# Performance work log

Measured on AMD Instinct MI355X. Metric: run time of the kernel, lower is better.

The kernel has to match this reference:

```python
import math
import jax, jax.numpy as jnp
import numpy as np

L, B, E, NDIM = 4096, 4, 1024, 16


def setup_inputs() -> dict:
    key = jax.random.key(0)
    ks = jax.random.split(key, 6)
    x = jax.random.normal(ks[0], (L, B, E), dtype=jnp.float32)
    alpha = jax.random.normal(ks[1], (2 * E, NDIM, 1), dtype=jnp.float32) * 0.2
    delta = jax.random.normal(ks[2], (2 * E, NDIM, 1), dtype=jnp.float32) * 0.2
    # beta init: N(0, 0.02) + alternating +-1 along ndim
    val = np.ones((NDIM, 1), dtype=np.float32)
    val[1::2] = -1.0
    beta = jax.random.normal(ks[3], (2 * E, NDIM, 1), dtype=jnp.float32) * 0.02 + jnp.asarray(val)
    gamma = jax.random.normal(ks[4], (2 * E, NDIM), dtype=jnp.float32)
    omega = jax.random.normal(ks[5], (E,), dtype=jnp.float32)
    return {"x": x, "alpha": alpha, "delta": delta, "beta": beta, "gamma": gamma, "omega": omega}


def reference(x, alpha, delta, beta, gamma, omega):
    seq_len, bsz, embed_dim = x.shape
    ndim = alpha.shape[1]
    scale = math.sqrt(1.0 / ndim)

    residual = x * omega  # (L, B, E)
    xc = jnp.transpose(x, (1, 2, 0))  # (B, E, L)

    a = jax.nn.sigmoid(alpha)
    d = jax.nn.sigmoid(delta)
    q = 1.0 - a * d          # (2E, ndim, 1)
    p = a * beta             # (2E, ndim, 1)

    t = jnp.arange(seq_len, dtype=x.dtype)          # (L,)
    vander = t[None, None, :] * jnp.log(q)          # (2E, ndim, L)
    kernel = p * jnp.exp(vander)                    # (2E, ndim, L)
    k = jnp.einsum('dnl,dn->dl', kernel, gamma * scale)  # (2E, L)

    fft_len = 2 * seq_len  # seq_len + kernel_size (truncation=None)
    k1, k2 = k[:embed_dim], k[embed_dim:]
    # bidirectional + shift: causal part padded right, flipped anti-causal padded left
    kb = jnp.pad(k1, ((0, 0), (0, seq_len))) + jnp.pad(k2[:, ::-1], ((0, 0), (seq_len, 0)))  # (E, 2L)

    k_f = jnp.fft.rfft(kb, n=fft_len)   # (E, L+1) complex
    x_f = jnp.fft.rfft(xc, n=fft_len)   # (B, E, L+1) complex
    out = jnp.fft.irfft(x_f * k_f, n=fft_len)[..., :seq_len]  # (B, E, L)
    out = out.astype(x.dtype)

    return jax.nn.silu(jnp.transpose(out, (2, 0, 1)) + residual)  # (L, B, E)
```

## Files before the change

kernel.cpp:

```cpp
#include <hip/hip_runtime.h>
#include <hip/hip_fp16.h>
#include <math.h>

#define L_  4096
#define B_  4
#define E_  1024
#define ND  16
#define CK  64
#define NC  (L_/CK)
#define BE  (B_*E_)
#define COLS (BE*ND)
#define CW  8

#define OFF_Q   0
#define OFF_W   (2*E_*ND)
#define OFF_QC  (2*2*E_*ND)
#define OFF_FS  (3*2*E_*ND)
#define OFF_GR  (OFF_FS + (size_t)NC*COLS)

__device__ __forceinline__ float sigm(float x){ return 1.0f/(1.0f+__expf(-x)); }

__global__ void k_params(const float* __restrict__ al,
                         const float* __restrict__ de,
                         const float* __restrict__ be,
                         const float* __restrict__ ga,
                         float* __restrict__ ws){
    int i = blockIdx.x*256 + threadIdx.x;
    float a = sigm(al[i]);
    float d = sigm(de[i]);
    float q = 1.0f - a*d;
    float w = a*be[i]*ga[i]*0.25f;
    float qc = q;
    #pragma unroll
    for(int k=0;k<6;k++) qc *= qc;
    ws[OFF_Q+i]=q; ws[OFF_W+i]=w; ws[OFF_QC+i]=qc;
}

__global__ __launch_bounds__(256) void k_summ(const float* __restrict__ x,
                                              float* __restrict__ ws){
    int bid = blockIdx.x;
    int c  = bid >> 4;
    int b  = (bid >> 2) & 3;
    int eg = bid & 3;
    int e  = eg*256 + threadIdx.x;
    const float* Q = ws + OFF_Q;
    float qf[ND], qb[ND], F[ND], G[ND];
    #pragma unroll
    for(int n=0;n<ND;n++){
        qf[n]=Q[e*ND+n]; qb[n]=Q[(E_+e)*ND+n]; F[n]=0.f; G[n]=0.f;
    }
    const float* xp = x + (size_t)(c*CK)*BE + b*E_ + e;
    #pragma unroll 16
    for(int i=0;i<CK;i++){
        float xa = xp[(size_t)i*BE];
        float xb = xp[(size_t)(CK-1-i)*BE];
        #pragma unroll
        for(int n=0;n<ND;n++){
            F[n]=fmaf(qf[n],F[n],xa);
            G[n]=fmaf(qb[n],G[n],xb);
        }
    }
    int col = (b*E_+e)*ND;
    float* Fp = ws + OFF_FS + (size_t)c*COLS + col;
    float* Gp = ws + OFF_GR + (size_t)c*COLS + col;
    #pragma unroll
    for(int n=0;n<ND;n++){ Fp[n]=F[n]; Gp[n]=G[n]; }
}

__global__ __launch_bounds__(256) void k_out2(const float* __restrict__ x,
                                              const float* __restrict__ om,
                                              const float* __restrict__ ws,
                                              float* __restrict__ out){
    __shared__ __half part[CK*256];
    const int tid = threadIdx.x;
    const int bid = blockIdx.x;
    const int c  = bid >> 4;
    const int b  = (bid >> 2) & 3;
    const int eg = bid & 3;
    const int e  = eg*256 + tid;
    const float* Q = ws + OFF_Q;
    const float* W = ws + OFF_W;
    const float omg = om[e];
    const int col = (b*E_+e)*ND;
    const float* xp = x + (size_t)(c*CK)*BE + b*E_ + e;

    {
        float st[ND];
        {
            float pw[ND], qcf[ND];
            #pragma unroll
            for(int n=0;n<ND;n++){ st[n]=0.f; pw[n]=1.f; qcf[n]=ws[OFF_QC+e*ND+n]; }
            int jm = (c < CW) ? c : CW;
            for(int j=1;j<=jm;j++){
                const float4* Fp = (const float4*)(ws + OFF_FS + (size_t)(c-j)*COLS + col);
                #pragma unroll
                for(int v=0;v<4;v++){
                    float4 f = Fp[v];
                    st[4*v+0]=fmaf(pw[4*v+0],f.x,st[4*v+0]);
                    st[4*v+1]=fmaf(pw[4*v+1],f.y,st[4*v+1]);
                    st[4*v+2]=fmaf(pw[4*v+2],f.z,st[4*v+2]);
                    st[4*v+3]=fmaf(pw[4*v+3],f.w,st[4*v+3]);
                }
                #pragma unroll
                for(int n=0;n<ND;n++) pw[n]*=qcf[n];
            }
        }
        float q1[ND], w1[ND];
        #pragma unroll
        for(int n=0;n<ND;n++){ q1[n]=Q[e*ND+n]; w1[n]=W[e*ND+n]; }
        #pragma unroll 4
        for(int i=0;i<CK;i++){
            float xv = xp[(size_t)i*BE];
            float acc = xv*omg;
            #pragma unroll
            for(int n=0;n<ND;n++){ st[n]=fmaf(q1[n],st[n],xv); acc=fmaf(w1[n],st[n],acc); }
            part[i*256+tid] = __float2half_rn(acc);
        }
    }

    {
        float rt[ND];
        {
            float pw[ND], qcb[ND];
            #pragma unroll
            for(int n=0;n<ND;n++){ rt[n]=0.f; pw[n]=1.f; qcb[n]=ws[OFF_QC+(E_+e)*ND+n]; }
            int jm = NC-1-c; if(jm > CW) jm = CW;
            for(int j=1;j<=jm;j++){
                const float4* Gp = (const float4*)(ws + OFF_GR + (size_t)(c+j)*COLS + col);
                #pragma unroll
                for(int v=0;v<4;v++){
                    float4 g = Gp[v];
                    rt[4*v+0]=fmaf(pw[4*v+0],g.x,rt[4*v+0]);
                    rt[4*v+1]=fmaf(pw[4*v+1],g.y,rt[4*v+1]);
                    rt[4*v+2]=fmaf(pw[4*v+2],g.z,rt[4*v+2]);
                    rt[4*v+3]=fmaf(pw[4*v+3],g.w,rt[4*v+3]);
                }
                #pragma unroll
                for(int n=0;n<ND;n++) pw[n]*=qcb[n];
            }
        }
        float q2[ND], w2[ND];
        #pragma unroll
        for(int n=0;n<ND;n++){ q2[n]=Q[(E_+e)*ND+n]; w2[n]=W[(E_+e)*ND+n]; }
        float* op = out + (size_t)(c*CK)*BE + b*E_ + e;
        #pragma unroll 4
        for(int i=CK-1;i>=0;i--){
            float acc = __half2float(part[i*256+tid]);
            #pragma unroll
            for(int n=0;n<ND;n++) acc = fmaf(w2[n], rt[n], acc);
            float z = acc;
            op[(size_t)i*BE] = z / (1.0f + __expf(-z));
            float xv = xp[(size_t)i*BE];
            #pragma unroll
            for(int n=0;n<ND;n++) rt[n]=fmaf(q2[n],rt[n],xv);
        }
    }
}

extern "C" void kernel_launch(void* const* d_in, const int* in_sizes, int n_in,
                              void* d_out, int out_size, void* d_ws, size_t ws_size,
                              hipStream_t stream) {
    const float* x  = (const float*)d_in[0];
    const float* al = (const float*)d_in[1];
    const float* de = (const float*)d_in[2];
    const float* be = (const float*)d_in[3];
    const float* ga = (const float*)d_in[4];
    const float* om = (const float*)d_in[5];
    float* ws = (float*)d_ws;
    float* out = (float*)d_out;

    k_params<<<dim3((2*E_*ND)/256), dim3(256), 0, stream>>>(al, de, be, ga, ws);
    k_summ  <<<dim3(NC*B_*(E_/256)), dim3(256), 0, stream>>>(x, ws);
    k_out2  <<<dim3(NC*B_*(E_/256)), dim3(256), 0, stream>>>(x, om, ws, out);
}
```

Measured before the change: 182.2 us.

## Split state dimension across thread pairs and combine partial sums with shuffles

Each embedding channel is now handled by two threads, each owning half of the 16 SSM state dimensions, which doubles the block count and halves per-thread registers. Partial output contributions are combined with a lane-xor shuffle, and each thread of the pair writes alternating timesteps. Launch bounds request higher occupancy. In exchange, each pair reads x twice, there are extra shuffles per step, and a block-wide sync is added between the forward and backward passes.

```diff
diff --git a/kernel.cpp b/kernel.cpp
--- a/kernel.cpp
+++ b/kernel.cpp
@@ -6,6 +6,7 @@
 #define B_  4
 #define E_  1024
 #define ND  16
+#define NH  8
 #define CK  64
 #define NC  (L_/CK)
 #define BE  (B_*E_)
@@ -36,123 +37,137 @@
     ws[OFF_Q+i]=q; ws[OFF_W+i]=w; ws[OFF_QC+i]=qc;
 }
 
-__global__ __launch_bounds__(256) void k_summ(const float* __restrict__ x,
-                                              float* __restrict__ ws){
-    int bid = blockIdx.x;
-    int c  = bid >> 4;
-    int b  = (bid >> 2) & 3;
-    int eg = bid & 3;
-    int e  = eg*256 + threadIdx.x;
+__global__ __launch_bounds__(256,8) void k_summ(const float* __restrict__ x,
+                                                float* __restrict__ ws){
+    const int bid = blockIdx.x;
+    const int c  = bid >> 5;
+    const int b  = (bid >> 3) & 3;
+    const int eg = bid & 7;
+    const int el = threadIdx.x >> 1;
+    const int h  = threadIdx.x & 1;
+    const int e  = eg*128 + el;
     const float* Q = ws + OFF_Q;
-    float qf[ND], qb[ND], F[ND], G[ND];
+    const int pb = e*ND + NH*h;
+    float qf[NH], qb[NH], F[NH], G[NH];
     #pragma unroll
-    for(int n=0;n<ND;n++){
-        qf[n]=Q[e*ND+n]; qb[n]=Q[(E_+e)*ND+n]; F[n]=0.f; G[n]=0.f;
+    for(int n=0;n<NH;n++){
+        qf[n]=Q[pb+n]; qb[n]=Q[E_*ND+pb+n]; F[n]=0.f; G[n]=0.f;
     }
     const float* xp = x + (size_t)(c*CK)*BE + b*E_ + e;
-    #pragma unroll 16
+    #pragma unroll 8
     for(int i=0;i<CK;i++){
         float xa = xp[(size_t)i*BE];
         float xb = xp[(size_t)(CK-1-i)*BE];
         #pragma unroll
-        for(int n=0;n<ND;n++){
+        for(int n=0;n<NH;n++){
             F[n]=fmaf(qf[n],F[n],xa);
             G[n]=fmaf(qb[n],G[n],xb);
         }
     }
-    int col = (b*E_+e)*ND;
+    const int col = (b*E_+e)*ND + NH*h;
     float* Fp = ws + OFF_FS + (size_t)c*COLS + col;
     float* Gp = ws + OFF_GR + (size_t)c*COLS + col;
     #pragma unroll
-    for(int n=0;n<ND;n++){ Fp[n]=F[n]; Gp[n]=G[n]; }
+    for(int n=0;n<NH;n++){ Fp[n]=F[n]; Gp[n]=G[n]; }
 }
 
-__global__ __launch_bounds__(256) void k_out2(const float* __restrict__ x,
-                                              const float* __restrict__ om,
-                                              const float* __restrict__ ws,
-                                              float* __restrict__ out){
-    __shared__ __half part[CK*256];
+__global__ __launch_bounds__(256,8) void k_out2(const float* __restrict__ x,
+                                                const float* __restrict__ om,
+                                                const float* __restrict__ ws,
+                                                float* __restrict__ out){
+    __shared__ __half part[CK*128];
     const int tid = threadIdx.x;
     const int bid = blockIdx.x;
-    const int c  = bid >> 4;
-    const int b  = (bid >> 2) & 3;
-    const int eg = bid & 3;
-    const int e  = eg*256 + tid;
+    const int c  = bid >> 5;
+    const int b  = (bid >> 3) & 3;
+    const int eg = bid & 7;
+    const int el = tid >> 1;
+    const int h  = tid & 1;
+    const int e  = eg*128 + el;
     const float* Q = ws + OFF_Q;
     const float* W = ws + OFF_W;
-    const float omg = om[e];
-    const int col = (b*E_+e)*ND;
+    const int pb  = e*ND + NH*h;
+    const int col = (b*E_+e)*ND + NH*h;
+    float om_eff = om[e];
+    if(h) om_eff = 0.0f;
     const float* xp = x + (size_t)(c*CK)*BE + b*E_ + e;
 
+    float st[NH];
     {
-        float st[ND];
-        {
-            float pw[ND], qcf[ND];
+        float pw[NH], qcf[NH];
+        #pragma unroll
+        for(int n=0;n<NH;n++){ st[n]=0.f; pw[n]=1.f; qcf[n]=ws[OFF_QC+pb+n]; }
+        int jm = (c < CW) ? c : CW;
+        for(int j=1;j<=jm;j++){
+            const float4* Fp = (const float4*)(ws + OFF_FS + (size_t)(c-j)*COLS + col);
             #pragma unroll
-            for(int n=0;n<ND;n++){ st[n]=0.f; pw[n]=1.f; qcf[n]=ws[OFF_QC+e*ND+n]; }
-            int jm = (c < CW) ? c : CW;
-            for(int j=1;j<=jm;j++){
-                const float4* Fp = (const float4*)(ws + OFF_FS + (size_t)(c-j)*COLS + col);
-                #pragma unroll
-                for(int v=0;v<4;v++){
-                    float4 f = Fp[v];
-                    st[4*v+0]=fmaf(pw[4*v+0],f.x,st[4*v+0]);
-                    st[4*v+1]=fmaf(pw[4*v+1],f.y,st[4*v+1]);
-                    st[4*v+2]=fmaf(pw[4*v+2],f.z,st[4*v+2]);
-                    st[4*v+3]=fmaf(pw[4*v+3],f.w,st[4*v+3]);
-                }
-                #pragma unroll
-                for(int n=0;n<ND;n++) pw[n]*=qcf[n];
+            for(int v=0;v<2;v++){
+                float4 f = Fp[v];
+                st[4*v+0]=fmaf(pw[4*v+0],f.x,st[4*v+0]);
+                st[4*v+1]=fmaf(pw[4*v+1],f.y,st[4*v+1]);
+                st[4*v+2]=fmaf(pw[4*v+2],f.z,st[4*v+2]);
+                st[4*v+3]=fmaf(pw[4*v+3],f.w,st[4*v+3]);
             }
+            #pragma unroll
+            for(int n=0;n<NH;n++) pw[n]*=qcf[n];
         }
-        float q1[ND], w1[ND];
+    }
+    {
+        float q1[NH], w1[NH];
         #pragma unroll
-        for(int n=0;n<ND;n++){ q1[n]=Q[e*ND+n]; w1[n]=W[e*ND+n]; }
+        for(int n=0;n<NH;n++){ q1[n]=Q[pb+n]; w1[n]=W[pb+n]; }
         #pragma unroll 4
         for(int i=0;i<CK;i++){
             float xv = xp[(size_t)i*BE];
-            float acc = xv*omg;
             #pragma unroll
-            for(int n=0;n<ND;n++){ st[n]=fmaf(q1[n],st[n],xv); acc=fmaf(w1[n],st[n],acc); }
-            part[i*256+tid] = __float2half_rn(acc);
+            for(int n=0;n<NH;n++) st[n]=fmaf(q1[n],st[n],xv);
+            float a0 = xv*om_eff, a1 = 0.f;
+            #pragma unroll
+            for(int n=0;n<4;n++){ a0=fmaf(w1[n],st[n],a0); a1=fmaf(w1[n+4],st[n+4],a1); }
+            float ph = a0 + a1;
+            float tot = ph + __shfl_xor(ph, 1);
+            if((i&1)==h) part[i*128+el] = __float2half_rn(tot);
         }
     }
+    __syncthreads();
 
+    float rt[NH];
     {
-        float rt[ND];
-        {
-            float pw[ND], qcb[ND];
+        float pw[NH], qcb[NH];
+        #pragma unroll
+        for(int n=0;n<NH;n++){ rt[n]=0.f; pw[n]=1.f; qcb[n]=ws[OFF_QC+E_*ND+pb+n]; }
+        int jm = NC-1-c; if(jm > CW) jm = CW;
+        for(int j=1;j<=jm;j++){
+            const float4* Gp = (const float4*)(ws + OFF_GR + (size_t)(c+j)*COLS + col);
             #pragma unroll
-            for(int n=0;n<ND;n++){ rt[n]=0.f; pw[n]=1.f; qcb[n]=ws[OFF_QC+(E_+e)*ND+n]; }
-            int jm = NC-1-c; if(jm > CW) jm = CW;
-            for(int j=1;j<=jm;j++){
-                const float4* Gp = (const float4*)(ws + OFF_GR + (size_t)(c+j)*COLS + col);
-                #pragma unroll
-                for(int v=0;v<4;v++){
-                    float4 g = Gp[v];
-                    rt[4*v+0]=fmaf(pw[4*v+0],g.x,rt[4*v+0]);
-                    rt[4*v+1]=fmaf(pw[4*v+1],g.y,rt[4*v+1]);
-                    rt[4*v+2]=fmaf(pw[4*v+2],g.z,rt[4*v+2]);
-                    rt[4*v+3]=fmaf(pw[4*v+3],g.w,rt[4*v+3]);
-                }
-                #pragma unroll
-                for(int n=0;n<ND;n++) pw[n]*=qcb[n];
+            for(int v=0;v<2;v++){
+                float4 g = Gp[v];
+                rt[4*v+0]=fmaf(pw[4*v+0],g.x,rt[4*v+0]);
+                rt[4*v+1]=fmaf(pw[4*v+1],g.y,rt[4*v+1]);
+                rt[4*v+2]=fmaf(pw[4*v+2],g.z,rt[4*v+2]);
+                rt[4*v+3]=fmaf(pw[4*v+3],g.w,rt[4*v+3]);
             }
+            #pragma unroll
+            for(int n=0;n<NH;n++) pw[n]*=qcb[n];
         }
-        float q2[ND], w2[ND];
+    }
+    {
+        float q2[NH], w2[NH];
         #pragma unroll
-        for(int n=0;n<ND;n++){ q2[n]=Q[(E_+e)*ND+n]; w2[n]=W[(E_+e)*ND+n]; }
+        for(int n=0;n<NH;n++){ q2[n]=Q[E_*ND+pb+n]; w2[n]=W[E_*ND+pb+n]; }
         float* op = out + (size_t)(c*CK)*BE + b*E_ + e;
         #pragma unroll 4
         for(int i=CK-1;i>=0;i--){
-            float acc = __half2float(part[i*256+tid]);
+            float b0=0.f, b1=0.f;
             #pragma unroll
-            for(int n=0;n<ND;n++) acc = fmaf(w2[n], rt[n], acc);
-            float z = acc;
-            op[(size_t)i*BE] = z / (1.0f + __expf(-z));
+            for(int n=0;n<4;n++){ b0=fmaf(w2[n],rt[n],b0); b1=fmaf(w2[n+4],rt[n+4],b1); }
+            float bh = b0 + b1;
+            float btot = bh + __shfl_xor(bh, 1);
+            float z = __half2float(part[i*128+el]) + btot;
+            if((i&1)==h) op[(size_t)i*BE] = z / (1.0f + __expf(-z));
             float xv = xp[(size_t)i*BE];
             #pragma unroll
-            for(int n=0;n<ND;n++) rt[n]=fmaf(q2[n],rt[n],xv);
+            for(int n=0;n<NH;n++) rt[n]=fmaf(q2[n],rt[n],xv);
         }
     }
 }
@@ -170,6 +185,6 @@
     float* out = (float*)d_out;
 
     k_params<<<dim3((2*E_*ND)/256), dim3(256), 0, stream>>>(al, de, be, ga, ws);
-    k_summ  <<<dim3(NC*B_*(E_/256)), dim3(256), 0, stream>>>(x, ws);
-    k_out2  <<<dim3(NC*B_*(E_/256)), dim3(256), 0, stream>>>(x, om, ws, out);
+    k_summ  <<<dim3(NC*B_*(E_/128)), dim3(256), 0, stream>>>(x, ws);
+    k_out2  <<<dim3(NC*B_*(E_/128)), dim3(256), 0, stream>>>(x, om, ws, out);
 }
```

Result: slower. 228.5 us (+25.4%).

## Template chunk size to 32 with halved lookback and single-pass summaries

Applied to the files above, without the earlier changes.

Makes the chunk length and cross-chunk lookback window template parameters. The default path now uses 32-step chunks with a 4-chunk lookback when the workspace is large enough, and 64-step chunks with a 4-chunk lookback otherwise. The summary kernel now reads each x value once and computes the reverse-direction state as a power-weighted sum instead of a second strided read. Shorter chunks double the block count and shorten the serial recurrence per thread, but double the summary writes. The reduced lookback truncates the decay tail (q^128 instead of q^512), which could hurt accuracy for slowly decaying channels.

```diff
diff --git a/kernel.cpp b/kernel.cpp
--- a/kernel.cpp
+++ b/kernel.cpp
@@ -6,17 +6,13 @@
 #define B_  4
 #define E_  1024
 #define ND  16
-#define CK  64
-#define NC  (L_/CK)
 #define BE  (B_*E_)
 #define COLS (BE*ND)
-#define CW  8
 
 #define OFF_Q   0
 #define OFF_W   (2*E_*ND)
 #define OFF_QC  (2*2*E_*ND)
 #define OFF_FS  (3*2*E_*ND)
-#define OFF_GR  (OFF_FS + (size_t)NC*COLS)
 
 __device__ __forceinline__ float sigm(float x){ return 1.0f/(1.0f+__expf(-x)); }
 
@@ -24,53 +20,56 @@
                          const float* __restrict__ de,
                          const float* __restrict__ be,
                          const float* __restrict__ ga,
-                         float* __restrict__ ws){
+                         float* __restrict__ ws, int lg){
     int i = blockIdx.x*256 + threadIdx.x;
     float a = sigm(al[i]);
     float d = sigm(de[i]);
     float q = 1.0f - a*d;
     float w = a*be[i]*ga[i]*0.25f;
     float qc = q;
-    #pragma unroll
-    for(int k=0;k<6;k++) qc *= qc;
+    for(int k=0;k<lg;k++) qc *= qc;
     ws[OFF_Q+i]=q; ws[OFF_W+i]=w; ws[OFF_QC+i]=qc;
 }
 
-__global__ __launch_bounds__(256) void k_summ(const float* __restrict__ x,
-                                              float* __restrict__ ws){
-    int bid = blockIdx.x;
-    int c  = bid >> 4;
-    int b  = (bid >> 2) & 3;
-    int eg = bid & 3;
-    int e  = eg*256 + threadIdx.x;
+template<int CK>
+__global__ __launch_bounds__(256) void k_summ_t(const float* __restrict__ x,
+                                                float* __restrict__ ws){
+    const int bid = blockIdx.x;
+    const int c  = bid >> 4;
+    const int b  = (bid >> 2) & 3;
+    const int eg = bid & 3;
+    const int e  = eg*256 + threadIdx.x;
     const float* Q = ws + OFF_Q;
-    float qf[ND], qb[ND], F[ND], G[ND];
+    float qf[ND], qb[ND], F[ND], G[ND], pw[ND];
     #pragma unroll
     for(int n=0;n<ND;n++){
-        qf[n]=Q[e*ND+n]; qb[n]=Q[(E_+e)*ND+n]; F[n]=0.f; G[n]=0.f;
+        qf[n]=Q[e*ND+n]; qb[n]=Q[(E_+e)*ND+n];
+        F[n]=0.f; G[n]=0.f; pw[n]=1.f;
     }
     const float* xp = x + (size_t)(c*CK)*BE + b*E_ + e;
-    #pragma unroll 16
+    #pragma unroll 4
     for(int i=0;i<CK;i++){
-        float xa = xp[(size_t)i*BE];
-        float xb = xp[(size_t)(CK-1-i)*BE];
+        float xv = xp[(size_t)i*BE];
         #pragma unroll
         for(int n=0;n<ND;n++){
-            F[n]=fmaf(qf[n],F[n],xa);
-            G[n]=fmaf(qb[n],G[n],xb);
+            F[n]=fmaf(qf[n],F[n],xv);
+            G[n]=fmaf(pw[n],xv,G[n]);
+            pw[n]*=qb[n];
         }
     }
-    int col = (b*E_+e)*ND;
+    const int col = (b*E_+e)*ND;
     float* Fp = ws + OFF_FS + (size_t)c*COLS + col;
-    float* Gp = ws + OFF_GR + (size_t)c*COLS + col;
+    float* Gp = ws + OFF_FS + (size_t)(L_/CK)*COLS + (size_t)c*COLS + col;
     #pragma unroll
     for(int n=0;n<ND;n++){ Fp[n]=F[n]; Gp[n]=G[n]; }
 }
 
-__global__ __launch_bounds__(256) void k_out2(const float* __restrict__ x,
-                                              const float* __restrict__ om,
-                                              const float* __restrict__ ws,
-                                              float* __restrict__ out){
+template<int CK, int CW>
+__global__ __launch_bounds__(256) void k_out2_t(const float* __restrict__ x,
+                                                const float* __restrict__ om,
+                                                const float* __restrict__ ws,
+                                                float* __restrict__ out){
+    constexpr int NC = L_/CK;
     __shared__ __half part[CK*256];
     const int tid = threadIdx.x;
     const int bid = blockIdx.x;
@@ -83,6 +82,8 @@
     const float omg = om[e];
     const int col = (b*E_+e)*ND;
     const float* xp = x + (size_t)(c*CK)*BE + b*E_ + e;
+    const float* FS = ws + OFF_FS;
+    const float* GR = ws + OFF_FS + (size_t)NC*COLS;
 
     {
         float st[ND];
@@ -92,7 +93,7 @@
             for(int n=0;n<ND;n++){ st[n]=0.f; pw[n]=1.f; qcf[n]=ws[OFF_QC+e*ND+n]; }
             int jm = (c < CW) ? c : CW;
             for(int j=1;j<=jm;j++){
-                const float4* Fp = (const float4*)(ws + OFF_FS + (size_t)(c-j)*COLS + col);
+                const float4* Fp = (const float4*)(FS + (size_t)(c-j)*COLS + col);
                 #pragma unroll
                 for(int v=0;v<4;v++){
                     float4 f = Fp[v];
@@ -126,7 +127,7 @@
             for(int n=0;n<ND;n++){ rt[n]=0.f; pw[n]=1.f; qcb[n]=ws[OFF_QC+(E_+e)*ND+n]; }
             int jm = NC-1-c; if(jm > CW) jm = CW;
             for(int j=1;j<=jm;j++){
-                const float4* Gp = (const float4*)(ws + OFF_GR + (size_t)(c+j)*COLS + col);
+                const float4* Gp = (const float4*)(GR + (size_t)(c+j)*COLS + col);
                 #pragma unroll
                 for(int v=0;v<4;v++){
                     float4 g = Gp[v];
@@ -169,7 +170,14 @@
     float* ws = (float*)d_ws;
     float* out = (float*)d_out;
 
-    k_params<<<dim3((2*E_*ND)/256), dim3(256), 0, stream>>>(al, de, be, ga, ws);
-    k_summ  <<<dim3(NC*B_*(E_/256)), dim3(256), 0, stream>>>(x, ws);
-    k_out2  <<<dim3(NC*B_*(E_/256)), dim3(256), 0, stream>>>(x, om, ws, out);
+    size_t need32 = ((size_t)OFF_FS + 2*(size_t)(L_/32)*COLS) * sizeof(float);
+    if (ws_size >= need32) {
+        k_params<<<dim3((2*E_*ND)/256), dim3(256), 0, stream>>>(al, de, be, ga, ws, 5);
+        k_summ_t<32>   <<<dim3((L_/32)*B_*(E_/256)), dim3(256), 0, stream>>>(x, ws);
+        k_out2_t<32,4> <<<dim3((L_/32)*B_*(E_/256)), dim3(256), 0, stream>>>(x, om, ws, out);
+    } else {
+        k_params<<<dim3((2*E_*ND)/256), dim3(256), 0, stream>>>(al, de, be, ga, ws, 6);
+        k_summ_t<64>   <<<dim3((L_/64)*B_*(E_/256)), dim3(256), 0, stream>>>(x, ws);
+        k_out2_t<64,4> <<<dim3((L_/64)*B_*(E_/256)), dim3(256), 0, stream>>>(x, om, ws, out);
+    }
 }
```

New measurement: 191.7 us. 5.2% more time.

## Use packed FP32 FMA for recurrences and shrink cross-chunk carry window

Applied to the files above, without the earlier changes.

Rewrites the per-state recurrences in both kernels with v_pk_fma_f32/v_pk_mul_f32 inline asm on float2 pairs, halving the VALU instruction count for the 16-state loops. The carry-in window drops from eight to two previous chunks, unrolled as direct loads. k_summ now computes the backward summary in the forward direction using a running power of q (G += q^i·x), which removes the reversed x load. The shorter window truncates more of the decaying kernel and may change accuracy. The dot products are split across two packed accumulators, which reorders the floating-point sums.

```diff
diff --git a/kernel.cpp b/kernel.cpp
--- a/kernel.cpp
+++ b/kernel.cpp
@@ -10,13 +10,19 @@
 #define NC  (L_/CK)
 #define BE  (B_*E_)
 #define COLS (BE*ND)
-#define CW  8
+#define CW  2
 
 #define OFF_Q   0
 #define OFF_W   (2*E_*ND)
 #define OFF_QC  (2*2*E_*ND)
 #define OFF_FS  (3*2*E_*ND)
 #define OFF_GR  (OFF_FS + (size_t)NC*COLS)
+
+typedef float v2f __attribute__((ext_vector_type(2)));
+
+#define PKFMA(d,s0,s1) asm("v_pk_fma_f32 %0, %1, %2, %0" : "+v"(d) : "v"(s0), "v"(s1))
+#define PKMAD(d,s0,s1) asm("v_pk_fma_f32 %0, %1, %0, %2" : "+v"(d) : "v"(s0), "v"(s1))
+#define PKMUL(d,s0)    asm("v_pk_mul_f32 %0, %1, %0"     : "+v"(d) : "v"(s0))
 
 __device__ __forceinline__ float sigm(float x){ return 1.0f/(1.0f+__expf(-x)); }
 
@@ -38,33 +44,36 @@
 
 __global__ __launch_bounds__(256) void k_summ(const float* __restrict__ x,
                                               float* __restrict__ ws){
-    int bid = blockIdx.x;
-    int c  = bid >> 4;
-    int b  = (bid >> 2) & 3;
-    int eg = bid & 3;
-    int e  = eg*256 + threadIdx.x;
-    const float* Q = ws + OFF_Q;
-    float qf[ND], qb[ND], F[ND], G[ND];
+    const int bid = blockIdx.x;
+    const int c  = bid >> 4;
+    const int b  = (bid >> 2) & 3;
+    const int eg = bid & 3;
+    const int e  = eg*256 + threadIdx.x;
+    const v2f* Qf = (const v2f*)(ws + OFF_Q + e*ND);
+    const v2f* Qb = (const v2f*)(ws + OFF_Q + (E_+e)*ND);
+    v2f qf[8], qb[8], F[8], G[8], pw[8];
     #pragma unroll
-    for(int n=0;n<ND;n++){
-        qf[n]=Q[e*ND+n]; qb[n]=Q[(E_+e)*ND+n]; F[n]=0.f; G[n]=0.f;
+    for(int k=0;k<8;k++){
+        qf[k]=Qf[k]; qb[k]=Qb[k];
+        F[k]=(v2f){0.f,0.f}; G[k]=(v2f){0.f,0.f}; pw[k]=(v2f){1.f,1.f};
     }
     const float* xp = x + (size_t)(c*CK)*BE + b*E_ + e;
-    #pragma unroll 16
+    #pragma unroll 4
     for(int i=0;i<CK;i++){
-        float xa = xp[(size_t)i*BE];
-        float xb = xp[(size_t)(CK-1-i)*BE];
+        float xv = xp[(size_t)i*BE];
+        v2f xx = {xv, xv};
         #pragma unroll
-        for(int n=0;n<ND;n++){
-            F[n]=fmaf(qf[n],F[n],xa);
-            G[n]=fmaf(qb[n],G[n],xb);
+        for(int k=0;k<8;k++){
+            PKMAD(F[k], qf[k], xx);
+            PKFMA(G[k], pw[k], xx);
+            PKMUL(pw[k], qb[k]);
         }
     }
-    int col = (b*E_+e)*ND;
-    float* Fp = ws + OFF_FS + (size_t)c*COLS + col;
-    float* Gp = ws + OFF_GR + (size_t)c*COLS + col;
+    const int col = (b*E_+e)*ND;
+    v2f* Fp = (v2f*)(ws + OFF_FS + (size_t)c*COLS + col);
+    v2f* Gp = (v2f*)(ws + OFF_GR + (size_t)c*COLS + col);
     #pragma unroll
-    for(int n=0;n<ND;n++){ Fp[n]=F[n]; Gp[n]=G[n]; }
+    for(int k=0;k<8;k++){ Fp[k]=F[k]; Gp[k]=G[k]; }
 }
 
 __global__ __launch_bounds__(256) void k_out2(const float* __restrict__ x,
@@ -78,81 +87,80 @@
     const int b  = (bid >> 2) & 3;
     const int eg = bid & 3;
     const int e  = eg*256 + tid;
-    const float* Q = ws + OFF_Q;
-    const float* W = ws + OFF_W;
     const float omg = om[e];
     const int col = (b*E_+e)*ND;
     const float* xp = x + (size_t)(c*CK)*BE + b*E_ + e;
 
     {
-        float st[ND];
+        v2f st[8];
         {
-            float pw[ND], qcf[ND];
+            const v2f* QC = (const v2f*)(ws + OFF_QC + e*ND);
             #pragma unroll
-            for(int n=0;n<ND;n++){ st[n]=0.f; pw[n]=1.f; qcf[n]=ws[OFF_QC+e*ND+n]; }
-            int jm = (c < CW) ? c : CW;
-            for(int j=1;j<=jm;j++){
-                const float4* Fp = (const float4*)(ws + OFF_FS + (size_t)(c-j)*COLS + col);
+            for(int k=0;k<8;k++) st[k]=(v2f){0.f,0.f};
+            if(c>=2){
+                const v2f* F2 = (const v2f*)(ws + OFF_FS + (size_t)(c-2)*COLS + col);
                 #pragma unroll
-                for(int v=0;v<4;v++){
-                    float4 f = Fp[v];
-                    st[4*v+0]=fmaf(pw[4*v+0],f.x,st[4*v+0]);
-                    st[4*v+1]=fmaf(pw[4*v+1],f.y,st[4*v+1]);
-                    st[4*v+2]=fmaf(pw[4*v+2],f.z,st[4*v+2]);
-                    st[4*v+3]=fmaf(pw[4*v+3],f.w,st[4*v+3]);
-                }
+                for(int k=0;k<8;k++) st[k]=F2[k];
+            }
+            if(c>=1){
+                const v2f* F1 = (const v2f*)(ws + OFF_FS + (size_t)(c-1)*COLS + col);
                 #pragma unroll
-                for(int n=0;n<ND;n++) pw[n]*=qcf[n];
+                for(int k=0;k<8;k++){ v2f qc=QC[k]; v2f f1=F1[k]; PKMAD(st[k], qc, f1); }
             }
         }
-        float q1[ND], w1[ND];
+        v2f q1[8], w1[8];
+        const v2f* Q1 = (const v2f*)(ws + OFF_Q + e*ND);
+        const v2f* W1 = (const v2f*)(ws + OFF_W + e*ND);
         #pragma unroll
-        for(int n=0;n<ND;n++){ q1[n]=Q[e*ND+n]; w1[n]=W[e*ND+n]; }
+        for(int k=0;k<8;k++){ q1[k]=Q1[k]; w1[k]=W1[k]; }
         #pragma unroll 4
         for(int i=0;i<CK;i++){
             float xv = xp[(size_t)i*BE];
-            float acc = xv*omg;
+            v2f xx = {xv, xv};
             #pragma unroll
-            for(int n=0;n<ND;n++){ st[n]=fmaf(q1[n],st[n],xv); acc=fmaf(w1[n],st[n],acc); }
+            for(int k=0;k<8;k++) PKMAD(st[k], q1[k], xx);
+            v2f aA={0.f,0.f}, aB={0.f,0.f};
+            #pragma unroll
+            for(int k=0;k<4;k++){ PKFMA(aA, w1[k], st[k]); PKFMA(aB, w1[k+4], st[k+4]); }
+            float acc = fmaf(xv, omg, (aA[0]+aA[1]) + (aB[0]+aB[1]));
             part[i*256+tid] = __float2half_rn(acc);
         }
     }
 
     {
-        float rt[ND];
+        v2f rt[8];
         {
-            float pw[ND], qcb[ND];
+            const v2f* QC = (const v2f*)(ws + OFF_QC + (E_+e)*ND);
             #pragma unroll
-            for(int n=0;n<ND;n++){ rt[n]=0.f; pw[n]=1.f; qcb[n]=ws[OFF_QC+(E_+e)*ND+n]; }
-            int jm = NC-1-c; if(jm > CW) jm = CW;
-            for(int j=1;j<=jm;j++){
-                const float4* Gp = (const float4*)(ws + OFF_GR + (size_t)(c+j)*COLS + col);
+            for(int k=0;k<8;k++) rt[k]=(v2f){0.f,0.f};
+            if(c<=NC-3){
+                const v2f* G2 = (const v2f*)(ws + OFF_GR + (size_t)(c+2)*COLS + col);
                 #pragma unroll
-                for(int v=0;v<4;v++){
-                    float4 g = Gp[v];
-                    rt[4*v+0]=fmaf(pw[4*v+0],g.x,rt[4*v+0]);
-                    rt[4*v+1]=fmaf(pw[4*v+1],g.y,rt[4*v+1]);
-                    rt[4*v+2]=fmaf(pw[4*v+2],g.z,rt[4*v+2]);
-                    rt[4*v+3]=fmaf(pw[4*v+3],g.w,rt[4*v+3]);
-                }
+                for(int k=0;k<8;k++) rt[k]=G2[k];
+            }
+            if(c<=NC-2){
+                const v2f* G1 = (const v2f*)(ws + OFF_GR + (size_t)(c+1)*COLS + col);
                 #pragma unroll
-                for(int n=0;n<ND;n++) pw[n]*=qcb[n];
+                for(int k=0;k<8;k++){ v2f qc=QC[k]; v2f g1=G1[k]; PKMAD(rt[k], qc, g1); }
             }
         }
-        float q2[ND], w2[ND];
+        v2f q2[8], w2[8];
+        const v2f* Q2 = (const v2f*)(ws + OFF_Q + (E_+e)*ND);
+        const v2f* W2 = (const v2f*)(ws + OFF_W + (E_+e)*ND);
         #pragma unroll
-        for(int n=0;n<ND;n++){ q2[n]=Q[(E_+e)*ND+n]; w2[n]=W[(E_+e)*ND+n]; }
+        for(int k=0;k<8;k++){ q2[k]=Q2[k]; w2[k]=W2[k]; }
         float* op = out + (size_t)(c*CK)*BE + b*E_ + e;
         #pragma unroll 4
         for(int i=CK-1;i>=0;i--){
-            float acc = __half2float(part[i*256+tid]);
+            v2f aA={0.f,0.f}, aB={0.f,0.f};
             #pragma unroll
-            for(int n=0;n<ND;n++) acc = fmaf(w2[n], rt[n], acc);
-            float z = acc;
+            for(int k=0;k<4;k++){ PKFMA(aA, w2[k], rt[k]); PKFMA(aB, w2[k+4], rt[k+4]); }
+            float z = __half2float(part[i*256+tid]) + (aA[0]+aA[1]) + (aB[0]+aB[1]);
             op[(size_t)i*BE] = z / (1.0f + __expf(-z));
             float xv = xp[(size_t)i*BE];
+            v2f xx = {xv, xv};
             #pragma unroll
-            for(int n=0;n<ND;n++) rt[n]=fmaf(q2[n],rt[n],xv);
+            for(int k=0;k<8;k++) PKMAD(rt[k], q2[k], xx);
         }
     }
 }
```

Result: slower. 186.8 us (+2.5%).
